# Performance work log

Measured on AMD Instinct MI355X. Metric: run time of the kernel, lower is better.

Reference implementation:

```python
import jax, jax.numpy as jnp
import numpy as np

T, H, E, K = 256, 2048, 60, 4          # tokens, hidden, num_experts, top_k
F, FS = 1408, 5632                      # moe_intermediate, shared_expert_intermediate


def setup_inputs() -> dict:
    key = jax.random.key(0)
    ks = jax.random.split(key, 9)
    s = 0.02  # weight init scale to keep activations sane
    return {
        "hidden_states": jax.random.normal(ks[0], (T, H), jnp.float32),
        "gate_w": jax.random.normal(ks[1], (H, E), jnp.float32) * s,       # router
        "w_gate": jax.random.normal(ks[2], (E, H, F), jnp.float32) * s,    # expert gate proj
        "w_up": jax.random.normal(ks[3], (E, H, F), jnp.float32) * s,      # expert up proj
        "w_down": jax.random.normal(ks[4], (E, F, H), jnp.float32) * s,    # expert down proj
        "sw_gate": jax.random.normal(ks[5], (H, FS), jnp.float32) * s,     # shared expert gate proj
        "sw_up": jax.random.normal(ks[6], (H, FS), jnp.float32) * s,       # shared expert up proj
        "sw_down": jax.random.normal(ks[7], (FS, H), jnp.float32) * s,     # shared expert down proj
        "shared_gate_w": jax.random.normal(ks[8], (H, 1), jnp.float32) * s,  # shared expert sigmoid gate
    }


def reference(hidden_states, gate_w, w_gate, w_up, w_down, sw_gate, sw_up, sw_down, shared_gate_w):
    x = hidden_states                                  # [T, H]
    # --- router: softmax then top-k (DefaultMoeRoutingMethod, no renorm) ---
    probs = jax.nn.softmax(x @ gate_w, axis=-1)        # [T, E]
    vals, idx = jax.lax.top_k(probs, K)                # [T, K]
    tok = jnp.arange(x.shape[0])[:, None]
    comb = jnp.zeros_like(probs).at[tok, idx].set(vals)  # dense combine weights [T, E]
    # --- experts: gated SiLU MLP per expert, combine-weighted (down is linear,
    #     so scaling the pre-down activation by comb equals scaling the output) ---
    g = jnp.einsum('th,ehf->tef', x, w_gate)           # [T, E, F]
    u = jnp.einsum('th,ehf->tef', x, w_up)             # [T, E, F]
    a = (jax.nn.silu(g) * u) * comb[:, :, None]
    moe_out = jnp.einsum('tef,efh->th', a, w_down)     # [T, H]
    # --- shared expert with sigmoid gate ---
    sh = (jax.nn.silu(x @ sw_gate) * (x @ sw_up)) @ sw_down   # [T, H]
    sh = jax.nn.sigmoid(x @ shared_gate_w) * sh
    return moe_out + sh
```

## Files before the change

kernel.cpp:

```cpp
#include <hip/hip_runtime.h>
#include <hip/hip_bf16.h>
#include <stdint.h>

typedef unsigned short ushort_t;
typedef uint32_t u32;
typedef __attribute__((ext_vector_type(8))) __bf16 bf16x8;
typedef __attribute__((ext_vector_type(8))) unsigned short u16x8;
typedef __attribute__((ext_vector_type(4))) float f32x4;

#define T_  256
#define H_  2048
#define E_  60
#define F_  1408
#define FS_ 5632

__device__ __forceinline__ u32 rne2(float lo, float hi){
  u32 a = __builtin_bit_cast(u32, lo);
  u32 b = __builtin_bit_cast(u32, hi);
  a += 0x7FFFu + ((a >> 16) & 1u);
  b += 0x7FFFu + ((b >> 16) & 1u);
  return (a >> 16) | (b & 0xFFFF0000u);
}
__device__ __forceinline__ ushort_t rne1(float f){
  u32 a = __builtin_bit_cast(u32, f);
  a += 0x7FFFu + ((a >> 16) & 1u);
  return (ushort_t)(a >> 16);
}
__device__ __forceinline__ f32x4 zero4(){ f32x4 z; z[0]=0.f; z[1]=0.f; z[2]=0.f; z[3]=0.f; return z; }

__device__ __forceinline__ bf16x8 ldsbS(const float* p, const int S){
  union { u32 u[4]; bf16x8 v; } cv;
  cv.u[0] = rne2(p[0],   p[S]);
  cv.u[1] = rne2(p[2*S], p[3*S]);
  cv.u[2] = rne2(p[4*S], p[5*S]);
  cv.u[3] = rne2(p[6*S], p[7*S]);
  return cv.v;
}
__device__ __forceinline__ bf16x8 loada(const ushort_t* p){
  return __builtin_bit_cast(bf16x8, *(const u16x8*)p);
}
__device__ __forceinline__ void gload16(const float* g, float* l){
  __builtin_amdgcn_global_load_lds(
      (const __attribute__((address_space(1))) void*)g,
      (__attribute__((address_space(3))) void*)l, 16, 0, 0);
}
#define MFMA(a,b,c) __builtin_amdgcn_mfma_f32_16x16x32_bf16((a),(b),(c),0,0,0)

#define VMW(n)  asm volatile("s_waitcnt vmcnt(" #n ")" ::: "memory")
#define BARM()  asm volatile("s_barrier" ::: "memory")
#define SCH()   __builtin_amdgcn_sched_barrier(0)

__global__ __launch_bounds__(256) void k_router(
    const float* __restrict__ x, const float* __restrict__ gw,
    const float* __restrict__ sgw, ushort_t* __restrict__ xb,
    int* __restrict__ tk_idx, float* __restrict__ tk_val, float* __restrict__ sig)
{
  const int t = blockIdx.x, tid = threadIdx.x;
  const float* xr = x + (size_t)t * H_;
  {
    const float4 v0 = *(const float4*)(xr + tid*8);
    const float4 v1 = *(const float4*)(xr + tid*8 + 4);
    u32* dst = (u32*)(xb + (size_t)t*H_ + tid*8);
    dst[0] = rne2(v0.x, v0.y); dst[1] = rne2(v0.z, v0.w);
    dst[2] = rne2(v1.x, v1.y); dst[3] = rne2(v1.z, v1.w);
  }
  __shared__ float s_part[4][64];
  __shared__ float s_logit[64];
  __shared__ float s_red[256];
  const int e = tid & 63, q = tid >> 6;
  float p = 0.f;
  if (e < E_) {
    const float* g = gw + e;
    for (int h = q*512; h < q*512 + 512; ++h) p += xr[h] * g[h*E_];
  }
  s_part[q][e] = p;
  float sp = 0.f;
  for (int h = tid; h < H_; h += 256) sp += xr[h] * sgw[h];
  s_red[tid] = sp;
  __syncthreads();
  if (tid < 64) s_logit[tid] = s_part[0][tid] + s_part[1][tid] + s_part[2][tid] + s_part[3][tid];
  for (int s = 128; s > 0; s >>= 1) {
    if (tid < s) s_red[tid] += s_red[tid + s];
    __syncthreads();
  }
  if (tid == 0) {
    sig[t] = 1.f / (1.f + expf(-s_red[0]));
    float mx = -3.4e38f;
    for (int i = 0; i < E_; ++i) mx = fmaxf(mx, s_logit[i]);
    float sum = 0.f;
    for (int i = 0; i < E_; ++i) sum += expf(s_logit[i] - mx);
    for (int k = 0; k < 4; ++k) {
      float bv = -3.4e38f; int bi = 0;
      for (int i = 0; i < E_; ++i) { float v = s_logit[i]; if (v > bv) { bv = v; bi = i; } }
      tk_idx[t*4 + k] = bi;
      tk_val[t*4 + k] = expf(bv - mx) / sum;
      s_logit[bi] = -3.4e38f;
    }
  }
}

__global__ __launch_bounds__(256) void k_lists(
    const int* __restrict__ tk_idx, const float* __restrict__ tk_val,
    int* __restrict__ cnt, int* __restrict__ ltok,
    int* __restrict__ lpair, float* __restrict__ lwt)
{
  __shared__ int   s_idx[1024];
  __shared__ float s_val[1024];
  const int tid = threadIdx.x;
  for (int i = tid; i < 1024; i += 256) { s_idx[i] = tk_idx[i]; s_val[i] = tk_val[i]; }
  __syncthreads();
  const int e = tid;
  if (e >= E_) return;
  int c = 0;
  for (int i = 0; i < 1024; ++i) {
    if (s_idx[i] == e && c < 64) {
      ltok[e*64 + c]  = i >> 2;
      lpair[e*64 + c] = i;
      lwt[e*64 + c]   = s_val[i];
      ++c;
    }
  }
  cnt[e] = c;
}

__global__ __launch_bounds__(256) void k_moe_gu(
    const ushort_t* __restrict__ xb, const float* __restrict__ wg_all,
    const float* __restrict__ wu_all, const int* __restrict__ cnt,
    const int* __restrict__ ltok, const float* __restrict__ lwt,
    ushort_t* __restrict__ act)
{
  __shared__ float lds[2][2*32*64];
  const int e = blockIdx.y;
  int m = cnt[e];
  if (m == 0) return;
  if (m > 64) m = 64;
  const int tid = threadIdx.x, wave = tid >> 6, lane = tid & 63;
  const int ln15 = lane & 15, kg = lane >> 4;
  const int col0 = blockIdx.x * 64;
  const size_t wbase = (size_t)e * ((size_t)H_ * F_) + col0;
  const float* gsg = wg_all + wbase + (size_t)(lane >> 4) * F_ + (lane & 15) * 4;
  const float* gsu = wu_all + wbase + (size_t)(lane >> 4) * F_ + (lane & 15) * 4;
  const int r0 = wave * 8;

  const ushort_t* ap[4];
  #pragma unroll
  for (int rt = 0; rt < 4; ++rt) {
    int row = rt*16 + ln15;
    int tok = ltok[e*64 + (row < m ? row : m-1)];
    ap[rt] = xb + (size_t)tok * H_ + kg*8;
  }

  f32x4 ag[4], au[4];
  #pragma unroll
  for (int i = 0; i < 4; ++i) { ag[i] = zero4(); au[i] = zero4(); }
  bf16x8 a0[4], a1[4];

#define GU_STAGE(B, K0) do { \
    gload16(gsg + (size_t)(K0 + r0)     * F_, &lds[B][r0*64]); \
    gload16(gsg + (size_t)(K0 + r0 + 4) * F_, &lds[B][(r0+4)*64]); \
    gload16(gsu + (size_t)(K0 + r0)     * F_, &lds[B][2048 + r0*64]); \
    gload16(gsu + (size_t)(K0 + r0 + 4) * F_, &lds[B][2048 + (r0+4)*64]); \
  } while(0)
#define GU_ALOAD(D, K0) do { \
    _Pragma("unroll") for (int rt = 0; rt < 4; ++rt) D[rt] = loada(ap[rt] + (K0)); } while(0)
#define GU_COMPUTE(B, A) do { \
    const float* lg_ = &lds[B][kg*512 + wave*16 + ln15]; \
    bf16x8 bg_ = ldsbS(lg_, 64); \
    bf16x8 bu_ = ldsbS(lg_ + 2048, 64); \
    _Pragma("unroll") for (int rt = 0; rt < 4; ++rt) { \
      ag[rt] = MFMA(A[rt], bg_, ag[rt]); \
      au[rt] = MFMA(A[rt], bu_, au[rt]); \
    } } while(0)

  GU_ALOAD(a0, 0);  GU_STAGE(0, 0);
  GU_ALOAD(a1, 32); GU_STAGE(1, 32);
  for (int t = 0; t + 2 < 64; t += 2) {
    VMW(8); BARM(); SCH();
    GU_COMPUTE(0, a0);
    BARM();
    GU_ALOAD(a0, (t+2)*32); GU_STAGE(0, (t+2)*32);
    VMW(8); BARM(); SCH();
    GU_COMPUTE(1, a1);
    BARM();
    GU_ALOAD(a1, (t+3)*32); GU_STAGE(1, (t+3)*32);
  }
  VMW(8); BARM(); SCH();
  GU_COMPUTE(0, a0);
  VMW(0); BARM(); SCH();
  GU_COMPUTE(1, a1);

  #pragma unroll
  for (int rt = 0; rt < 4; ++rt)
    #pragma unroll
    for (int j = 0; j < 4; ++j) {
      int r = rt*16 + kg*4 + j;
      if (r < m) {
        float wt = lwt[e*64 + r];
        float g = ag[rt][j], u = au[rt][j];
        float a = g / (1.f + __expf(-g)) * u * wt;
        act[((size_t)e*64 + r) * F_ + col0 + wave*16 + ln15] = rne1(a);
      }
    }
}

__global__ __launch_bounds__(256) void k_moe_down(
    const ushort_t* __restrict__ act, const float* __restrict__ wd_all,
    const int* __restrict__ cnt, const int* __restrict__ lpair,
    float* __restrict__ out4)
{
  __shared__ float lds[2][32*64];
  __shared__ int s_pair[64];
  const int e = blockIdx.y;
  int m = cnt[e];
  if (m == 0) return;
  if (m > 64) m = 64;
  const int tid = threadIdx.x, wave = tid >> 6, lane = tid & 63;
  const int ln15 = lane & 15, kg = lane >> 4;
  if (tid < 64) s_pair[tid] = (tid < m) ? lpair[e*64 + tid] : 0;
  const int col0 = blockIdx.x * 64;
  const float* gsd = wd_all + (size_t)e * ((size_t)F_ * H_) + col0
                   + (size_t)(lane >> 4) * H_ + (lane & 15) * 4;
  const int r0 = wave * 8;

  const ushort_t* ap[4];
  #pragma unroll
  for (int rt = 0; rt < 4; ++rt)
    ap[rt] = act + ((size_t)e*64 + rt*16 + ln15) * F_ + kg*8;

  f32x4 ac[4];
  #pragma unroll
  for (int i = 0; i < 4; ++i) ac[i] = zero4();
  bf16x8 a0[4], a1[4];

#define DN_STAGE(B, K0) do { \
    gload16(gsd + (size_t)(K0 + r0)     * H_, &lds[B][r0*64]); \
    gload16(gsd + (size_t)(K0 + r0 + 4) * H_, &lds[B][(r0+4)*64]); \
  } while(0)
#define DN_ALOAD(D, K0) do { \
    _Pragma("unroll") for (int rt = 0; rt < 4; ++rt) D[rt] = loada(ap[rt] + (K0)); } while(0)
#define DN_COMPUTE(B, A) do { \
    const float* lw_ = &lds[B][kg*512 + wave*16 + ln15]; \
    bf16x8 b_ = ldsbS(lw_, 64); \
    _Pragma("unroll") for (int rt = 0; rt < 4; ++rt) \
      ac[rt] = MFMA(A[rt], b_, ac[rt]); \
  } while(0)

  DN_ALOAD(a0, 0);  DN_STAGE(0, 0);
  DN_ALOAD(a1, 32); DN_STAGE(1, 32);
  for (int t = 0; t + 2 < 44; t += 2) {
    VMW(6); BARM(); SCH();
    DN_COMPUTE(0, a0);
    BARM();
    DN_ALOAD(a0, (t+2)*32); DN_STAGE(0, (t+2)*32);
    VMW(6); BARM(); SCH();
    DN_COMPUTE(1, a1);
    BARM();
    DN_ALOAD(a1, (t+3)*32); DN_STAGE(1, (t+3)*32);
  }
  VMW(6); BARM(); SCH();
  DN_COMPUTE(0, a0);
  VMW(0); BARM(); SCH();
  DN_COMPUTE(1, a1);

  #pragma unroll
  for (int rt = 0; rt < 4; ++rt)
    #pragma unroll
    for (int j = 0; j < 4; ++j) {
      int r = rt*16 + kg*4 + j;
      if (r < m)
        out4[(size_t)s_pair[r] * H_ + col0 + wave*16 + ln15] = ac[rt][j];
    }
}

__global__ __launch_bounds__(256) void k_sh_gu(
    const ushort_t* __restrict__ xb, const float* __restrict__ swg,
    const float* __restrict__ swu, ushort_t* __restrict__ acts)
{
  __shared__ float lds[2][2048];
  const int tid = threadIdx.x, wave = tid >> 6, lane = tid & 63;
  const int ln15 = lane & 15, kg = lane >> 4;
  const int cb = blockIdx.x * 32;
  const int rowb = wave * 64;
  const int r0 = wave * 8;
  const float* gsg = swg + (size_t)(lane >> 3) * FS_ + cb + (lane & 7) * 4;
  const float* gsu = swu + (size_t)(lane >> 3) * FS_ + cb + (lane & 7) * 4;

  const ushort_t* ap[4];
  #pragma unroll
  for (int rt = 0; rt < 4; ++rt)
    ap[rt] = xb + (size_t)(rowb + rt*16 + ln15) * H_ + kg*8;

  f32x4 ag[4][2], au[4][2];
  #pragma unroll
  for (int i = 0; i < 4; ++i) { ag[i][0]=zero4(); ag[i][1]=zero4(); au[i][0]=zero4(); au[i][1]=zero4(); }
  bf16x8 a0[4], a1[4];

#define SG_STAGE(B, K0) do { \
    gload16(gsg + (size_t)(K0 + r0) * FS_, &lds[B][r0*32]); \
    gload16(gsu + (size_t)(K0 + r0) * FS_, &lds[B][1024 + r0*32]); \
  } while(0)
#define SG_ALOAD(D, K0) do { \
    _Pragma("unroll") for (int rt = 0; rt < 4; ++rt) D[rt] = loada(ap[rt] + (K0)); } while(0)
#define SG_COMPUTE(B, A) do { \
    const float* lg_ = &lds[B][kg*256 + ln15]; \
    bf16x8 bg0_ = ldsbS(lg_, 32), bg1_ = ldsbS(lg_ + 16, 32); \
    bf16x8 bu0_ = ldsbS(lg_ + 1024, 32), bu1_ = ldsbS(lg_ + 1040, 32); \
    _Pragma("unroll") for (int rt = 0; rt < 4; ++rt) { \
      ag[rt][0] = MFMA(A[rt], bg0_, ag[rt][0]); \
      ag[rt][1] = MFMA(A[rt], bg1_, ag[rt][1]); \
      au[rt][0] = MFMA(A[rt], bu0_, au[rt][0]); \
      au[rt][1] = MFMA(A[rt], bu1_, au[rt][1]); \
    } } while(0)

  SG_ALOAD(a0, 0);  SG_STAGE(0, 0);
  SG_ALOAD(a1, 32); SG_STAGE(1, 32);
  for (int t = 0; t + 2 < 64; t += 2) {
    VMW(6); BARM(); SCH();
    SG_COMPUTE(0, a0);
    BARM();
    SG_ALOAD(a0, (t+2)*32); SG_STAGE(0, (t+2)*32);
    VMW(6); BARM(); SCH();
    SG_COMPUTE(1, a1);
    BARM();
    SG_ALOAD(a1, (t+3)*32); SG_STAGE(1, (t+3)*32);
  }
  VMW(6); BARM(); SCH();
  SG_COMPUTE(0, a0);
  VMW(0); BARM(); SCH();
  SG_COMPUTE(1, a1);

  #pragma unroll
  for (int rt = 0; rt < 4; ++rt)
    #pragma unroll
    for (int nt = 0; nt < 2; ++nt)
      #pragma unroll
      for (int j = 0; j < 4; ++j) {
        int row = rowb + rt*16 + kg*4 + j;
        float g = ag[rt][nt][j], u = au[rt][nt][j];
        acts[(size_t)row * FS_ + cb + nt*16 + ln15] = rne1(g / (1.f + __expf(-g)) * u);
      }
}

__global__ __launch_bounds__(256) void k_sh_down(
    const ushort_t* __restrict__ acts, const float* __restrict__ swd,
    float* __restrict__ acc4)
{
  __shared__ float lds[2][2048];
  const int tid = threadIdx.x, wave = tid >> 6, lane = tid & 63;
  const int ln15 = lane & 15, kg = lane >> 4;
  const int cb = blockIdx.x * 64;
  const int kh = blockIdx.y;
  const int rowb = wave * 64;
  const int r0 = wave * 8;
  const float* gsd = swd + (size_t)(kh*1408) * H_ + cb
                   + (size_t)(lane >> 4) * H_ + (lane & 15) * 4;

  const ushort_t* ap[4];
  #pragma unroll
  for (int rt = 0; rt < 4; ++rt)
    ap[rt] = acts + (size_t)(rowb + rt*16 + ln15) * FS_ + kh*1408 + kg*8;

  f32x4 ac[4][4];
  #pragma unroll
  for (int i = 0; i < 4; ++i)
    #pragma unroll
    for (int c = 0; c < 4; ++c) ac[i][c] = zero4();
  bf16x8 a0[4], a1[4];

#define SD_STAGE(B, K0) do { \
    gload16(gsd + (size_t)(K0 + r0) * H_,     &lds[B][r0*64]); \
    gload16(gsd + (size_t)(K0 + r0 + 4) * H_, &lds[B][(r0+4)*64]); \
  } while(0)
#define SD_ALOAD(D, K0) do { \
    _Pragma("unroll") for (int rt = 0; rt < 4; ++rt) D[rt] = loada(ap[rt] + (K0)); } while(0)
#define SD_COMPUTE(B, A) do { \
    const float* lw_ = &lds[B][kg*512 + ln15]; \
    bf16x8 b0_ = ldsbS(lw_, 64),      b1_ = ldsbS(lw_ + 16, 64); \
    bf16x8 b2_ = ldsbS(lw_ + 32, 64), b3_ = ldsbS(lw_ + 48, 64); \
    _Pragma("unroll") for (int rt = 0; rt < 4; ++rt) { \
      ac[rt][0] = MFMA(A[rt], b0_, ac[rt][0]); \
      ac[rt][1] = MFMA(A[rt], b1_, ac[rt][1]); \
      ac[rt][2] = MFMA(A[rt], b2_, ac[rt][2]); \
      ac[rt][3] = MFMA(A[rt], b3_, ac[rt][3]); \
    } } while(0)

  SD_ALOAD(a0, 0);  SD_STAGE(0, 0);
  SD_ALOAD(a1, 32); SD_STAGE(1, 32);
  for (int t = 0; t + 2 < 44; t += 2) {
    VMW(6); BARM(); SCH();
    SD_COMPUTE(0, a0);
    BARM();
    SD_ALOAD(a0, (t+2)*32); SD_STAGE(0, (t+2)*32);
    VMW(6); BARM(); SCH();
    SD_COMPUTE(1, a1);
    BARM();
    SD_ALOAD(a1, (t+3)*32); SD_STAGE(1, (t+3)*32);
  }
  VMW(6); BARM(); SCH();
  SD_COMPUTE(0, a0);
  VMW(0); BARM(); SCH();
  SD_COMPUTE(1, a1);

  #pragma unroll
  for (int rt = 0; rt < 4; ++rt)
    #pragma unroll
    for (int c = 0; c < 4; ++c)
      #pragma unroll
      for (int j = 0; j < 4; ++j) {
        int row = rowb + rt*16 + kg*4 + j;
        acc4[((size_t)kh * T_ + row) * H_ + cb + c*16 + ln15] = ac[rt][c][j];
      }
}

__global__ __launch_bounds__(256) void k_final(
    const float* __restrict__ acc4, const float* __restrict__ out4,
    const float* __restrict__ sig, float* __restrict__ out)
{
  const int idx = blockIdx.x * blockDim.x + threadIdx.x;
  const int t = idx >> 9;
  const int h = (idx & 511) * 4;
  float ox = 0.f, oy = 0.f, oz = 0.f, ow = 0.f;
  #pragma unroll
  for (int s = 0; s < 4; ++s) {
    const float4 v = *(const float4*)(acc4 + ((size_t)s * T_ + t) * H_ + h);
    ox += v.x; oy += v.y; oz += v.z; ow += v.w;
  }
  const float sg = sig[t];
  ox *= sg; oy *= sg; oz *= sg; ow *= sg;
  #pragma unroll
  for (int k = 0; k < 4; ++k) {
    const float4 e4 = *(const float4*)(out4 + (size_t)(t*4 + k) * H_ + h);
    ox += e4.x; oy += e4.y; oz += e4.z; ow += e4.w;
  }
  float4 o; o.x = ox; o.y = oy; o.z = oz; o.w = ow;
  *(float4*)(out + (size_t)t * H_ + h) = o;
}

extern "C" void kernel_launch(void* const* d_in, const int* in_sizes, int n_in,
                              void* d_out, int out_size, void* d_ws, size_t ws_size,
                              hipStream_t stream)
{
  (void)in_sizes; (void)n_in; (void)out_size; (void)ws_size;
  const float* x   = (const float*)d_in[0];
  const float* gw  = (const float*)d_in[1];
  const float* wg  = (const float*)d_in[2];
  const float* wu  = (const float*)d_in[3];
  const float* wd  = (const float*)d_in[4];
  const float* swg = (const float*)d_in[5];
  const float* swu = (const float*)d_in[6];
  const float* swd = (const float*)d_in[7];
  const float* sgw = (const float*)d_in[8];

  char* ws = (char*)d_ws;
  ushort_t* xb    = (ushort_t*)(ws);
  ushort_t* act   = (ushort_t*)(ws + 1048576);
  ushort_t* acts  = (ushort_t*)(ws + 11862016);
  float*    out4  = (float*)   (ws + 14745600);
  float*    acc4  = (float*)   (ws + 23134208);
  float*    sig   = (float*)   (ws + 31522816);
  int*      tkidx = (int*)     (ws + 31523840);
  float*    tkval = (float*)   (ws + 31527936);
  int*      cnt   = (int*)     (ws + 31532032);
  int*      ltok  = (int*)     (ws + 31532288);
  int*      lpair = (int*)     (ws + 31547648);
  float*    lwt   = (float*)   (ws + 31563008);

  k_router  <<<T_, 256, 0, stream>>>(x, gw, sgw, xb, tkidx, tkval, sig);
  k_lists   <<<1, 256, 0, stream>>>(tkidx, tkval, cnt, ltok, lpair, lwt);
  k_moe_gu  <<<dim3(F_/64, E_), 256, 0, stream>>>(xb, wg, wu, cnt, ltok, lwt, act);
  k_moe_down<<<dim3(H_/64, E_), 256, 0, stream>>>(act, wd, cnt, lpair, out4);
  k_sh_gu   <<<dim3(FS_/32), 256, 0, stream>>>(xb, swg, swu, acts);
  k_sh_down <<<dim3(H_/64, 4), 256, 0, stream>>>(acts, swd, acc4);
  k_final   <<<512, 256, 0, stream>>>(acc4, out4, sig, (float*)d_out);
}
```

Measured before the change: 716.3 us.

## Enlarge MoE expert GEMM tiles to 128 columns and 64-deep K stages with 512 threads

The expert gate/up and down kernels move from 64-column, 32-deep K tiles with 4 waves to 128-column, 64-deep K tiles with 8 waves per block. Each stage now loads twice as many rows and columns of fp32 weights into LDS, which halves the number of barrier-separated iterations, and the grid shrinks by half along the column dimension. The intent is to cut per-iteration sync and issue overhead and to raise bytes in flight per block while streaming the large fp32 expert weights. In exchange LDS use grows to 128KB for gate/up, which limits occupancy to one block per CU. The gate/up grid also drops to 11x60 blocks, which may leave some CUs idle.

After: 690.9 us. 3.5% less time.

```diff
diff --git a/kernel.cpp b/kernel.cpp
--- a/kernel.cpp
+++ b/kernel.cpp
@@ -123,24 +123,25 @@
   cnt[e] = c;
 }
 
-__global__ __launch_bounds__(256) void k_moe_gu(
+__global__ __launch_bounds__(512) void k_moe_gu(
     const ushort_t* __restrict__ xb, const float* __restrict__ wg_all,
     const float* __restrict__ wu_all, const int* __restrict__ cnt,
     const int* __restrict__ ltok, const float* __restrict__ lwt,
     ushort_t* __restrict__ act)
 {
-  __shared__ float lds[2][2*32*64];
+  __shared__ float lds[2][2*64*128];
   const int e = blockIdx.y;
   int m = cnt[e];
   if (m == 0) return;
   if (m > 64) m = 64;
   const int tid = threadIdx.x, wave = tid >> 6, lane = tid & 63;
   const int ln15 = lane & 15, kg = lane >> 4;
-  const int col0 = blockIdx.x * 64;
+  const int col0 = blockIdx.x * 128;
   const size_t wbase = (size_t)e * ((size_t)H_ * F_) + col0;
-  const float* gsg = wg_all + wbase + (size_t)(lane >> 4) * F_ + (lane & 15) * 4;
-  const float* gsu = wu_all + wbase + (size_t)(lane >> 4) * F_ + (lane & 15) * 4;
+  const float* gsg = wg_all + wbase + (size_t)(lane >> 5) * F_ + (lane & 31) * 4;
+  const float* gsu = wu_all + wbase + (size_t)(lane >> 5) * F_ + (lane & 31) * 4;
   const int r0 = wave * 8;
+  const int c0 = wave * 16;
 
   const ushort_t* ap[4];
   #pragma unroll
@@ -153,38 +154,43 @@
   f32x4 ag[4], au[4];
   #pragma unroll
   for (int i = 0; i < 4; ++i) { ag[i] = zero4(); au[i] = zero4(); }
-  bf16x8 a0[4], a1[4];
+  bf16x8 a0[4][2], a1[4][2];
 
 #define GU_STAGE(B, K0) do { \
-    gload16(gsg + (size_t)(K0 + r0)     * F_, &lds[B][r0*64]); \
-    gload16(gsg + (size_t)(K0 + r0 + 4) * F_, &lds[B][(r0+4)*64]); \
-    gload16(gsu + (size_t)(K0 + r0)     * F_, &lds[B][2048 + r0*64]); \
-    gload16(gsu + (size_t)(K0 + r0 + 4) * F_, &lds[B][2048 + (r0+4)*64]); \
-  } while(0)
+    _Pragma("unroll") for (int i2 = 0; i2 < 4; ++i2) { \
+      int r_ = r0 + i2*2; \
+      gload16(gsg + (size_t)(K0 + r_) * F_, &lds[B][r_*128]); \
+      gload16(gsu + (size_t)(K0 + r_) * F_, &lds[B][8192 + r_*128]); \
+    } } while(0)
 #define GU_ALOAD(D, K0) do { \
-    _Pragma("unroll") for (int rt = 0; rt < 4; ++rt) D[rt] = loada(ap[rt] + (K0)); } while(0)
+    _Pragma("unroll") for (int rt = 0; rt < 4; ++rt) { \
+      D[rt][0] = loada(ap[rt] + (K0)); \
+      D[rt][1] = loada(ap[rt] + (K0) + 32); \
+    } } while(0)
 #define GU_COMPUTE(B, A) do { \
-    const float* lg_ = &lds[B][kg*512 + wave*16 + ln15]; \
-    bf16x8 bg_ = ldsbS(lg_, 64); \
-    bf16x8 bu_ = ldsbS(lg_ + 2048, 64); \
-    _Pragma("unroll") for (int rt = 0; rt < 4; ++rt) { \
-      ag[rt] = MFMA(A[rt], bg_, ag[rt]); \
-      au[rt] = MFMA(A[rt], bu_, au[rt]); \
+    _Pragma("unroll") for (int kk = 0; kk < 2; ++kk) { \
+      const float* lg_ = &lds[B][(kk*32 + kg*8)*128 + c0 + ln15]; \
+      bf16x8 bg_ = ldsbS(lg_, 128); \
+      bf16x8 bu_ = ldsbS(lg_ + 8192, 128); \
+      _Pragma("unroll") for (int rt = 0; rt < 4; ++rt) { \
+        ag[rt] = MFMA(A[rt][kk], bg_, ag[rt]); \
+        au[rt] = MFMA(A[rt][kk], bu_, au[rt]); \
+      } \
     } } while(0)
 
   GU_ALOAD(a0, 0);  GU_STAGE(0, 0);
-  GU_ALOAD(a1, 32); GU_STAGE(1, 32);
-  for (int t = 0; t + 2 < 64; t += 2) {
-    VMW(8); BARM(); SCH();
+  GU_ALOAD(a1, 64); GU_STAGE(1, 64);
+  for (int t = 0; t + 2 < 32; t += 2) {
+    VMW(16); BARM(); SCH();
     GU_COMPUTE(0, a0);
     BARM();
-    GU_ALOAD(a0, (t+2)*32); GU_STAGE(0, (t+2)*32);
-    VMW(8); BARM(); SCH();
+    GU_ALOAD(a0, (t+2)*64); GU_STAGE(0, (t+2)*64);
+    VMW(16); BARM(); SCH();
     GU_COMPUTE(1, a1);
     BARM();
-    GU_ALOAD(a1, (t+3)*32); GU_STAGE(1, (t+3)*32);
-  }
-  VMW(8); BARM(); SCH();
+    GU_ALOAD(a1, (t+3)*64); GU_STAGE(1, (t+3)*64);
+  }
+  VMW(16); BARM(); SCH();
   GU_COMPUTE(0, a0);
   VMW(0); BARM(); SCH();
   GU_COMPUTE(1, a1);
@@ -198,17 +204,17 @@
         float wt = lwt[e*64 + r];
         float g = ag[rt][j], u = au[rt][j];
         float a = g / (1.f + __expf(-g)) * u * wt;
-        act[((size_t)e*64 + r) * F_ + col0 + wave*16 + ln15] = rne1(a);
+        act[((size_t)e*64 + r) * F_ + col0 + c0 + ln15] = rne1(a);
       }
     }
 }
 
-__global__ __launch_bounds__(256) void k_moe_down(
+__global__ __launch_bounds__(512) void k_moe_down(
     const ushort_t* __restrict__ act, const float* __restrict__ wd_all,
     const int* __restrict__ cnt, const int* __restrict__ lpair,
     float* __restrict__ out4)
 {
-  __shared__ float lds[2][32*64];
+  __shared__ float lds[2][64*128];
   __shared__ int s_pair[64];
   const int e = blockIdx.y;
   int m = cnt[e];
@@ -217,10 +223,11 @@
   const int tid = threadIdx.x, wave = tid >> 6, lane = tid & 63;
   const int ln15 = lane & 15, kg = lane >> 4;
   if (tid < 64) s_pair[tid] = (tid < m) ? lpair[e*64 + tid] : 0;
-  const int col0 = blockIdx.x * 64;
+  const int col0 = blockIdx.x * 128;
   const float* gsd = wd_all + (size_t)e * ((size_t)F_ * H_) + col0
-                   + (size_t)(lane >> 4) * H_ + (lane & 15) * 4;
+                   + (size_t)(lane >> 5) * H_ + (lane & 31) * 4;
   const int r0 = wave * 8;
+  const int c0 = wave * 16;
 
   const ushort_t* ap[4];
   #pragma unroll
@@ -230,34 +237,39 @@
   f32x4 ac[4];
   #pragma unroll
   for (int i = 0; i < 4; ++i) ac[i] = zero4();
-  bf16x8 a0[4], a1[4];
+  bf16x8 a0[4][2], a1[4][2];
 
 #define DN_STAGE(B, K0) do { \
-    gload16(gsd + (size_t)(K0 + r0)     * H_, &lds[B][r0*64]); \
-    gload16(gsd + (size_t)(K0 + r0 + 4) * H_, &lds[B][(r0+4)*64]); \
-  } while(0)
+    _Pragma("unroll") for (int i2 = 0; i2 < 4; ++i2) { \
+      int r_ = r0 + i2*2; \
+      gload16(gsd + (size_t)(K0 + r_) * H_, &lds[B][r_*128]); \
+    } } while(0)
 #define DN_ALOAD(D, K0) do { \
-    _Pragma("unroll") for (int rt = 0; rt < 4; ++rt) D[rt] = loada(ap[rt] + (K0)); } while(0)
+    _Pragma("unroll") for (int rt = 0; rt < 4; ++rt) { \
+      D[rt][0] = loada(ap[rt] + (K0)); \
+      D[rt][1] = loada(ap[rt] + (K0) + 32); \
+    } } while(0)
 #define DN_COMPUTE(B, A) do { \
-    const float* lw_ = &lds[B][kg*512 + wave*16 + ln15]; \
-    bf16x8 b_ = ldsbS(lw_, 64); \
-    _Pragma("unroll") for (int rt = 0; rt < 4; ++rt) \
-      ac[rt] = MFMA(A[rt], b_, ac[rt]); \
-  } while(0)
+    _Pragma("unroll") for (int kk = 0; kk < 2; ++kk) { \
+      const float* lw_ = &lds[B][(kk*32 + kg*8)*128 + c0 + ln15]; \
+      bf16x8 b_ = ldsbS(lw_, 128); \
+      _Pragma("unroll") for (int rt = 0; rt < 4; ++rt) \
+        ac[rt] = MFMA(A[rt][kk], b_, ac[rt]); \
+    } } while(0)
 
   DN_ALOAD(a0, 0);  DN_STAGE(0, 0);
-  DN_ALOAD(a1, 32); DN_STAGE(1, 32);
-  for (int t = 0; t + 2 < 44; t += 2) {
-    VMW(6); BARM(); SCH();
+  DN_ALOAD(a1, 64); DN_STAGE(1, 64);
+  for (int t = 0; t + 2 < 22; t += 2) {
+    VMW(12); BARM(); SCH();
     DN_COMPUTE(0, a0);
     BARM();
-    DN_ALOAD(a0, (t+2)*32); DN_STAGE(0, (t+2)*32);
-    VMW(6); BARM(); SCH();
+    DN_ALOAD(a0, (t+2)*64); DN_STAGE(0, (t+2)*64);
+    VMW(12); BARM(); SCH();
     DN_COMPUTE(1, a1);
     BARM();
-    DN_ALOAD(a1, (t+3)*32); DN_STAGE(1, (t+3)*32);
-  }
-  VMW(6); BARM(); SCH();
+    DN_ALOAD(a1, (t+3)*64); DN_STAGE(1, (t+3)*64);
+  }
+  VMW(12); BARM(); SCH();
   DN_COMPUTE(0, a0);
   VMW(0); BARM(); SCH();
   DN_COMPUTE(1, a1);
@@ -268,7 +280,7 @@
     for (int j = 0; j < 4; ++j) {
       int r = rt*16 + kg*4 + j;
       if (r < m)
-        out4[(size_t)s_pair[r] * H_ + col0 + wave*16 + ln15] = ac[rt][j];
+        out4[(size_t)s_pair[r] * H_ + col0 + c0 + ln15] = ac[rt][j];
     }
 }
 
@@ -467,8 +479,8 @@
 
   k_router  <<<T_, 256, 0, stream>>>(x, gw, sgw, xb, tkidx, tkval, sig);
   k_lists   <<<1, 256, 0, stream>>>(tkidx, tkval, cnt, ltok, lpair, lwt);
-  k_moe_gu  <<<dim3(F_/64, E_), 256, 0, stream>>>(xb, wg, wu, cnt, ltok, lwt, act);
-  k_moe_down<<<dim3(H_/64, E_), 256, 0, stream>>>(act, wd, cnt, lpair, out4);
+  k_moe_gu  <<<dim3(F_/128, E_), 512, 0, stream>>>(xb, wg, wu, cnt, ltok, lwt, act);
+  k_moe_down<<<dim3(H_/128, E_), 512, 0, stream>>>(act, wd, cnt, lpair, out4);
   k_sh_gu   <<<dim3(FS_/32), 256, 0, stream>>>(xb, swg, swu, acts);
   k_sh_down <<<dim3(H_/64, 4), 256, 0, stream>>>(acts, swd, acc4);
   k_final   <<<512, 256, 0, stream>>>(acc4, out4, sig, (float*)d_out);
```
